# Kernel tuning notes

Measured on AMD Instinct MI355X. Metric: run time of the kernel, lower is better.

Reference implementation:

```python
import jax, jax.numpy as jnp
import numpy as np

B, T, I, H, C = 4096, 512, 3, 32, 3  # batch, seq_len, input, hidden, classes


def setup_inputs() -> dict:
    key = jax.random.key(0)
    ks = jax.random.split(key, 7)
    s = 1.0 / np.sqrt(H)  # PyTorch LSTM init scale
    return {
        "x": jax.random.normal(ks[0], (B, T, I), dtype=jnp.float32),
        "W_ih": jax.random.normal(ks[1], (4 * H, I), dtype=jnp.float32) * s,
        "W_hh": jax.random.normal(ks[2], (4 * H, H), dtype=jnp.float32) * s,
        "b_ih": jax.random.normal(ks[3], (4 * H,), dtype=jnp.float32) * s,
        "b_hh": jax.random.normal(ks[4], (4 * H,), dtype=jnp.float32) * s,
        "W_fc": jax.random.normal(ks[5], (C, H), dtype=jnp.float32) * s,
        "b_fc": jax.random.normal(ks[6], (C,), dtype=jnp.float32) * s,
    }


def reference(x, W_ih, W_hh, b_ih, b_hh, W_fc, b_fc):
    # Precompute input contribution to all gates for every timestep: (B,T,4H)
    xg = jnp.einsum("bti,gi->btg", x, W_ih) + b_ih + b_hh
    h0 = jnp.zeros((x.shape[0], H), dtype=x.dtype)
    c0 = jnp.zeros_like(h0)

    def step(carry, xt):
        h, c = carry
        g = xt + h @ W_hh.T  # (B,4H)
        i_g, f_g, g_g, o_g = jnp.split(g, 4, axis=-1)  # PyTorch gate order i,f,g,o
        i_g = jax.nn.sigmoid(i_g)
        f_g = jax.nn.sigmoid(f_g)
        g_g = jnp.tanh(g_g)
        o_g = jax.nn.sigmoid(o_g)
        c = f_g * c + i_g * g_g
        h = o_g * jnp.tanh(c)
        return (h, c), None

    (h_last, _), _ = jax.lax.scan(step, (h0, c0), jnp.swapaxes(xg, 0, 1))
    return h_last @ W_fc.T + b_fc  # (B, num_classes)
```

## Files before the change

### kernel.cpp

```cpp
#include <hip/hip_runtime.h>
#include <cstdint>

#define B_TOT 4096
#define T_LEN 512
#define CHUNK 128
#define LOG2E 1.44269504088896340736f
#define HSTR  40

typedef _Float16 f16x8 __attribute__((ext_vector_type(8)));
typedef _Float16 f16x4 __attribute__((ext_vector_type(4)));
typedef float    f32x4 __attribute__((ext_vector_type(4)));

__device__ __forceinline__ float ex2(float v)  { return __builtin_amdgcn_exp2f(v); }
__device__ __forceinline__ float rcp_(float v) { return __builtin_amdgcn_rcpf(v); }

__global__ __launch_bounds__(512, 2)
void lstm_w8(const float* __restrict__ x,
             const float* __restrict__ W_ih,
             const float* __restrict__ W_hh,
             const float* __restrict__ b_ih,
             const float* __restrict__ b_hh,
             const float* __restrict__ W_fc,
             const float* __restrict__ b_fc,
             float* __restrict__ out)
{
    __shared__ __align__(16) _Float16 hbuf[2][16][HSTR];
    __shared__ __align__(16) _Float16 xbuf[CHUNK][16][4];

    const int tid  = threadIdx.x;
    const int wave = tid >> 6;
    const int lane = tid & 63;
    const int n    = lane & 15;
    const int kq   = lane >> 4;
    const int tb   = blockIdx.x * 16;

    const int   gate_m = n & 3;
    const int   hid_m  = 4 * wave + (n >> 2);
    const int   Rm     = gate_m * 32 + hid_m;
    const float sm     = (gate_m == 2) ? (-2.0f * LOG2E) : (-LOG2E);

    f16x8 aW;
#pragma unroll
    for (int j = 0; j < 8; ++j)
        aW[j] = (_Float16)(sm * W_hh[Rm * 32 + 8 * kq + j]);

    f16x8 a2 = {};
    if (kq == 0) {
        a2[0] = (_Float16)(sm * W_ih[Rm * 3 + 0]);
        a2[1] = (_Float16)(sm * W_ih[Rm * 3 + 1]);
        a2[2] = (_Float16)(sm * W_ih[Rm * 3 + 2]);
        a2[3] = (_Float16)(sm * (b_ih[Rm] + b_hh[Rm]));
    }

    const int hid_s = 4 * wave + kq;

    {
        int* hz = (int*)&hbuf[0][0][0];
        for (int i = tid; i < (2 * 16 * HSTR) / 2; i += 512) hz[i] = 0;
    }

    float c = 0.0f;
    f32x4 accx;

    for (int tc = 0; tc < T_LEN; tc += CHUNK) {
#pragma unroll
        for (int s = 0; s < 4; ++s) {
            const int idx = tid + s * 512;
            const int tl = idx >> 4, m = idx & 15;
            const float* xp = x + ((size_t)(tb + m) * T_LEN + (tc + tl)) * 3;
            f16x4 v;
            v[0] = (_Float16)xp[0]; v[1] = (_Float16)xp[1];
            v[2] = (_Float16)xp[2]; v[3] = (_Float16)1.0f;
            *(f16x4*)&xbuf[tl][m][0] = v;
        }
        __syncthreads();

        {
            const f16x4 xv = *(const f16x4*)&xbuf[0][n][0];
            f16x8 b2 = {};
            if (kq == 0) { b2[0] = xv[0]; b2[1] = xv[1]; b2[2] = xv[2]; b2[3] = xv[3]; }
            accx = f32x4{0.f, 0.f, 0.f, 0.f};
            accx = __builtin_amdgcn_mfma_f32_16x16x32_f16(a2, b2, accx, 0, 0, 0);
        }

#pragma unroll 2
        for (int tt = 0; tt < CHUNK; ++tt) {
            const int p = tt & 1;

            const f16x8 bh  = *(const f16x8*)&hbuf[p][n][8 * kq];
            const f32x4 acc = __builtin_amdgcn_mfma_f32_16x16x32_f16(aW, bh, accx, 0, 0, 0);

            const float iv = rcp_(1.0f + ex2(acc[0]));
            const float fv = rcp_(1.0f + ex2(acc[1]));
            const float gv = fmaf(2.0f, rcp_(1.0f + ex2(acc[2])), -1.0f);
            const float ov = rcp_(1.0f + ex2(acc[3]));

            c = fmaf(fv, c, iv * gv);
            const float th = fmaf(2.0f, rcp_(1.0f + ex2(c * (-2.0f * LOG2E))), -1.0f);
            const float h  = ov * th;

            hbuf[p ^ 1][n][hid_s] = (_Float16)h;

            const int ttn = (tt + 1 < CHUNK) ? (tt + 1) : 0;
            const f16x4 xv = *(const f16x4*)&xbuf[ttn][n][0];
            f16x8 b2 = {};
            if (kq == 0) { b2[0] = xv[0]; b2[1] = xv[1]; b2[2] = xv[2]; b2[3] = xv[3]; }
            accx = f32x4{0.f, 0.f, 0.f, 0.f};
            accx = __builtin_amdgcn_mfma_f32_16x16x32_f16(a2, b2, accx, 0, 0, 0);

            __syncthreads();
        }
    }

    if (tid < 48) {
        const int m = tid / 3, cc = tid % 3;
        float acc = b_fc[cc];
#pragma unroll
        for (int k = 0; k < 32; ++k)
            acc = fmaf(W_fc[cc * 32 + k], (float)hbuf[0][m][k], acc);
        out[(tb + m) * 3 + cc] = acc;
    }
}

extern "C" void kernel_launch(void* const* d_in, const int* in_sizes, int n_in,
                              void* d_out, int out_size, void* d_ws, size_t ws_size,
                              hipStream_t stream) {
    const float* x    = (const float*)d_in[0];
    const float* W_ih = (const float*)d_in[1];
    const float* W_hh = (const float*)d_in[2];
    const float* b_ih = (const float*)d_in[3];
    const float* b_hh = (const float*)d_in[4];
    const float* W_fc = (const float*)d_in[5];
    const float* b_fc = (const float*)d_in[6];
    float* out = (float*)d_out;

    dim3 grid(B_TOT / 16);
    dim3 block(512);
    lstm_w8<<<grid, block, 0, stream>>>(x, W_ih, W_hh, b_ih, b_hh, W_fc, b_fc, out);
}
```

Measured before the change: 205.6 us.

## Switch LSTM recurrence to 32x32x16 MFMA with 4 waves and fused gate math

Replaces the 8-wave 16x16x32 MFMA layout with 4 waves, each issuing two 32x32x16 MFMAs per step over a 32-row gate tile, with two hidden units per lane. The gate nonlinearities are rewritten algebraically so several reciprocals merge into fewer rcp calls per cell update. The aim is to halve the threads taking part in each per-step barrier and to cut transcendental work on the serial critical path. The cost is more work per lane, longer MFMA latency per step, and launch bounds of 256x1, which may reduce occupancy.

Result: slower. 215.8 us (+4.9%).

```diff
diff --git a/kernel.cpp b/kernel.cpp
--- a/kernel.cpp
+++ b/kernel.cpp
@@ -7,15 +7,16 @@
 #define LOG2E 1.44269504088896340736f
 #define HSTR  40
 
-typedef _Float16 f16x8 __attribute__((ext_vector_type(8)));
-typedef _Float16 f16x4 __attribute__((ext_vector_type(4)));
-typedef float    f32x4 __attribute__((ext_vector_type(4)));
+typedef _Float16 f16x8  __attribute__((ext_vector_type(8)));
+typedef _Float16 f16x4  __attribute__((ext_vector_type(4)));
+typedef float    f32x4  __attribute__((ext_vector_type(4)));
+typedef float    f32x16 __attribute__((ext_vector_type(16)));
 
 __device__ __forceinline__ float ex2(float v)  { return __builtin_amdgcn_exp2f(v); }
 __device__ __forceinline__ float rcp_(float v) { return __builtin_amdgcn_rcpf(v); }
 
-__global__ __launch_bounds__(512, 2)
-void lstm_w8(const float* __restrict__ x,
+__global__ __launch_bounds__(256, 1)
+void lstm_32(const float* __restrict__ x,
              const float* __restrict__ W_ih,
              const float* __restrict__ W_hh,
              const float* __restrict__ b_ih,
@@ -30,42 +31,44 @@
     const int tid  = threadIdx.x;
     const int wave = tid >> 6;
     const int lane = tid & 63;
-    const int n    = lane & 15;
-    const int kq   = lane >> 4;
+    const int c    = lane & 31;
+    const int hi   = lane >> 5;
+    const int nb   = c & 15;
+    const int sel  = (c >> 4) & 1;
     const int tb   = blockIdx.x * 16;
 
-    const int   gate_m = n & 3;
-    const int   hid_m  = 4 * wave + (n >> 2);
-    const int   Rm     = gate_m * 32 + hid_m;
+    const int   gate_m = c & 3;
+    const int   Rm     = gate_m * 32 + 8 * wave + (c >> 2);
     const float sm     = (gate_m == 2) ? (-2.0f * LOG2E) : (-LOG2E);
 
-    f16x8 aW;
+    f16x8 aK0, aK1;
 #pragma unroll
-    for (int j = 0; j < 8; ++j)
-        aW[j] = (_Float16)(sm * W_hh[Rm * 32 + 8 * kq + j]);
-
+    for (int j = 0; j < 8; ++j) {
+        aK0[j] = (_Float16)(sm * W_hh[Rm * 32 +      8 * hi + j]);
+        aK1[j] = (_Float16)(sm * W_hh[Rm * 32 + 16 + 8 * hi + j]);
+    }
     f16x8 a2 = {};
-    if (kq == 0) {
+    if (hi == 0) {
         a2[0] = (_Float16)(sm * W_ih[Rm * 3 + 0]);
         a2[1] = (_Float16)(sm * W_ih[Rm * 3 + 1]);
         a2[2] = (_Float16)(sm * W_ih[Rm * 3 + 2]);
         a2[3] = (_Float16)(sm * (b_ih[Rm] + b_hh[Rm]));
     }
 
-    const int hid_s = 4 * wave + kq;
+    const int hidA = 8 * wave + 4 * sel + hi;
+    const int hidB = hidA + 2;
 
-    {
-        int* hz = (int*)&hbuf[0][0][0];
-        for (int i = tid; i < (2 * 16 * HSTR) / 2; i += 512) hz[i] = 0;
-    }
+    for (int i = tid; i < 320; i += 256) ((int*)&hbuf[0][0][0])[i] = 0;
 
-    float c = 0.0f;
-    f32x4 accx;
+    const float K2 = -2.0f * LOG2E;
+    float cA = 0.0f, cB = 0.0f;
+    const f32x16 z = {0.f};
+    f32x16 accx;
 
     for (int tc = 0; tc < T_LEN; tc += CHUNK) {
 #pragma unroll
-        for (int s = 0; s < 4; ++s) {
-            const int idx = tid + s * 512;
+        for (int s = 0; s < 8; ++s) {
+            const int idx = tid + s * 256;
             const int tl = idx >> 4, m = idx & 15;
             const float* xp = x + ((size_t)(tb + m) * T_LEN + (tc + tl)) * 3;
             f16x4 v;
@@ -76,37 +79,59 @@
         __syncthreads();
 
         {
-            const f16x4 xv = *(const f16x4*)&xbuf[0][n][0];
+            const f16x4 xv = *(const f16x4*)&xbuf[0][nb][0];
             f16x8 b2 = {};
-            if (kq == 0) { b2[0] = xv[0]; b2[1] = xv[1]; b2[2] = xv[2]; b2[3] = xv[3]; }
-            accx = f32x4{0.f, 0.f, 0.f, 0.f};
-            accx = __builtin_amdgcn_mfma_f32_16x16x32_f16(a2, b2, accx, 0, 0, 0);
+            if (hi == 0) { b2[0] = xv[0]; b2[1] = xv[1]; b2[2] = xv[2]; b2[3] = xv[3]; }
+            accx = __builtin_amdgcn_mfma_f32_32x32x16_f16(a2, b2, z, 0, 0, 0);
         }
 
 #pragma unroll 2
         for (int tt = 0; tt < CHUNK; ++tt) {
             const int p = tt & 1;
 
-            const f16x8 bh  = *(const f16x8*)&hbuf[p][n][8 * kq];
-            const f32x4 acc = __builtin_amdgcn_mfma_f32_16x16x32_f16(aW, bh, accx, 0, 0, 0);
+            const f16x8 bh0 = *(const f16x8*)&hbuf[p][nb][8 * hi];
+            const f16x8 bh1 = *(const f16x8*)&hbuf[p][nb][16 + 8 * hi];
+            const int ttn = (tt + 1) & (CHUNK - 1);
+            const f16x4 xvN = *(const f16x4*)&xbuf[ttn][nb][0];
 
-            const float iv = rcp_(1.0f + ex2(acc[0]));
-            const float fv = rcp_(1.0f + ex2(acc[1]));
-            const float gv = fmaf(2.0f, rcp_(1.0f + ex2(acc[2])), -1.0f);
-            const float ov = rcp_(1.0f + ex2(acc[3]));
+            f32x16 ac = __builtin_amdgcn_mfma_f32_32x32x16_f16(aK0, bh0, accx, 0, 0, 0);
+            ac        = __builtin_amdgcn_mfma_f32_32x32x16_f16(aK1, bh1, ac,   0, 0, 0);
 
-            c = fmaf(fv, c, iv * gv);
-            const float th = fmaf(2.0f, rcp_(1.0f + ex2(c * (-2.0f * LOG2E))), -1.0f);
-            const float h  = ov * th;
+            const f32x4 q0lo = __builtin_shufflevector(ac, ac, 0, 1, 2, 3);
+            const f32x4 q1lo = __builtin_shufflevector(ac, ac, 4, 5, 6, 7);
+            const f32x4 q0hi = __builtin_shufflevector(ac, ac, 8, 9, 10, 11);
+            const f32x4 q1hi = __builtin_shufflevector(ac, ac, 12, 13, 14, 15);
+            const f32x4 qA = sel ? q0hi : q0lo;
+            const f32x4 qB = sel ? q1hi : q1lo;
 
-            hbuf[p ^ 1][n][hid_s] = (_Float16)h;
+            float hA, hB;
+            {
+                const float ei = ex2(qA[0]), ef = ex2(qA[1]), eg = ex2(qA[2]), eo = ex2(qA[3]);
+                const float pi = 1.0f + ei, pf = 1.0f + ef, pg = 1.0f + eg;
+                const float mg = 1.0f - eg;
+                const float pp = pi * pg, qn = mg * pf;
+                cA = fmaf(cA, pp, qn) * rcp_(pf * pp);
+                const float ec = ex2(cA * K2);
+                const float po = 1.0f + eo, pc = 1.0f + ec, mc = 1.0f - ec;
+                hA = mc * rcp_(po * pc);
+            }
+            {
+                const float ei = ex2(qB[0]), ef = ex2(qB[1]), eg = ex2(qB[2]), eo = ex2(qB[3]);
+                const float pi = 1.0f + ei, pf = 1.0f + ef, pg = 1.0f + eg;
+                const float mg = 1.0f - eg;
+                const float pp = pi * pg, qn = mg * pf;
+                cB = fmaf(cB, pp, qn) * rcp_(pf * pp);
+                const float ec = ex2(cB * K2);
+                const float po = 1.0f + eo, pc = 1.0f + ec, mc = 1.0f - ec;
+                hB = mc * rcp_(po * pc);
+            }
 
-            const int ttn = (tt + 1 < CHUNK) ? (tt + 1) : 0;
-            const f16x4 xv = *(const f16x4*)&xbuf[ttn][n][0];
+            hbuf[p ^ 1][nb][hidA] = (_Float16)hA;
+            hbuf[p ^ 1][nb][hidB] = (_Float16)hB;
+
             f16x8 b2 = {};
-            if (kq == 0) { b2[0] = xv[0]; b2[1] = xv[1]; b2[2] = xv[2]; b2[3] = xv[3]; }
-            accx = f32x4{0.f, 0.f, 0.f, 0.f};
-            accx = __builtin_amdgcn_mfma_f32_16x16x32_f16(a2, b2, accx, 0, 0, 0);
+            if (hi == 0) { b2[0] = xvN[0]; b2[1] = xvN[1]; b2[2] = xvN[2]; b2[3] = xvN[3]; }
+            accx = __builtin_amdgcn_mfma_f32_32x32x16_f16(a2, b2, z, 0, 0, 0);
 
             __syncthreads();
         }
@@ -135,6 +160,6 @@
     float* out = (float*)d_out;
 
     dim3 grid(B_TOT / 16);
-    dim3 block(512);
-    lstm_w8<<<grid, block, 0, stream>>>(x, W_ih, W_hh, b_ih, b_hh, W_fc, b_fc, out);
+    dim3 block(256);
+    lstm_32<<<grid, block, 0, stream>>>(x, W_ih, W_hh, b_ih, b_hh, W_fc, b_fc, out);
 }
```
